# Optimization experiments

Hardware: AMD Instinct MI355X
Metric: run time of the kernel (lower is better)

## Reference

```python
import jax, jax.numpy as jnp
import numpy as np

K, Q, DIM = 64, 128, 1024
TF_W, DE_W, FFT_W = 1.0, 0.8, 0.6  # opt.TF_weight / DE_weight / FFT_weight


def setup_inputs() -> dict:
    key = jax.random.key(0)
    ks = jax.random.split(key, 9)
    def feats(k):
        return jax.random.normal(k, (K, Q, DIM), dtype=jnp.float32)
    def protos(k):
        return jax.random.normal(k, (K, DIM), dtype=jnp.float32)
    def var(k):
        # positive variances, bounded away from zero
        return jax.random.uniform(k, (K,), dtype=jnp.float32) + 0.5
    return {
        "TFq_output": feats(ks[0]), "TFs_proto": protos(ks[1]), "TF_variance": var(ks[2]),
        "DEq_output": feats(ks[3]), "DEs_proto": protos(ks[4]), "DE_variance": var(ks[5]),
        "FFTq_output": feats(ks[6]), "FFTs_proto": protos(ks[7]), "FFT_variance": var(ks[8]),
    }


def _mah_dist(xq, proto, variance):
    # ||x - p||^2 / var via expansion: avoids materializing (num, protonum, dim)
    x2 = jnp.sum(xq * xq, axis=1, keepdims=True)            # (num, 1)
    p2 = jnp.sum(proto * proto, axis=1)[None, :]            # (1, protonum)
    xp = xq @ proto.T                                       # (num, protonum)
    return (x2 - 2.0 * xp + p2) / variance[None, :]


def _modality(xq, proto, variance, w):
    logits = -_mah_dist(xq, proto, variance)
    pred = w * jax.nn.softmax(logits, axis=1)
    mahloss = -(w * jax.nn.log_softmax(logits, axis=1))
    return pred, mahloss


def reference(TFq_output, TFs_proto, TF_variance,
              DEq_output, DEs_proto, DE_variance,
              FFTq_output, FFTs_proto, FFT_variance):
    k, q, _ = TFq_output.shape
    y = jnp.repeat(jnp.arange(k), q)                         # (k*q,)

    tf_pred, tf_loss = _modality(TFq_output.reshape(k * q, -1), TFs_proto, TF_variance, TF_W)
    de_pred, de_loss = _modality(DEq_output.reshape(k * q, -1), DEs_proto, DE_variance, DE_W)
    fft_pred, fft_loss = _modality(FFTq_output.reshape(k * q, -1), FFTs_proto, FFT_variance, FFT_W)

    fusion_loss = tf_loss + de_loss + fft_loss               # (k*q, k)
    loss = jnp.take_along_axis(fusion_loss, y[:, None], axis=1).squeeze(-1).mean()

    pred_mah = tf_pred + de_pred + fft_pred
    pred = jnp.argmax(pred_mah, axis=1)
    acc = (pred == y).astype(jnp.float32).mean()
    return (loss, acc)
```

## Files before the change

kernel.cpp:

```cpp
#include <hip/hip_runtime.h>


typedef _Float16 half8 __attribute__((ext_vector_type(8)));
typedef float    floatx4 __attribute__((ext_vector_type(4)));

#define NCLS   64
#define QPC    128
#define DIM    1024
#define NROWS  (NCLS * QPC)
#define NRT    (NROWS / 16)

#define OFF_W      0
#define W_BYTES    (3 * NCLS * DIM * 2)
#define OFF_P2     W_BYTES
#define OFF_LP     (OFF_P2 + 3 * NCLS * 4)
#define OFF_CP     (OFF_LP + NRT * 4)
#define WS_NEED    (OFF_CP + NRT * 4)

__device__ __forceinline__ void dma16(const float* g, float* l) {
    __builtin_amdgcn_global_load_lds(
        (const __attribute__((address_space(1))) void*)g,
        (__attribute__((address_space(3))) void*)l,
        16, 0, 0);
}

__global__ __launch_bounds__(64) void prep_protos(
    const float* __restrict__ Ptf, const float* __restrict__ Pde,
    const float* __restrict__ Pff, _Float16* __restrict__ W,
    float* __restrict__ p2)
{
    const int m    = blockIdx.x >> 5;
    const int kcg  = blockIdx.x & 31;
    const int lane = threadIdx.x;
    const int l15  = lane & 15;
    const int quad = lane >> 4;
    const float* __restrict__ P = (m == 0) ? Ptf : (m == 1) ? Pde : Pff;

    #pragma unroll
    for (int t = 0; t < 4; ++t) {
        const float* src = P + (size_t)(t * 16 + l15) * DIM + kcg * 32 + quad * 8;
        const float4 b0 = *reinterpret_cast<const float4*>(src);
        const float4 b1 = *reinterpret_cast<const float4*>(src + 4);
        half8 h;
        h[0] = (_Float16)b0.x; h[1] = (_Float16)b0.y;
        h[2] = (_Float16)b0.z; h[3] = (_Float16)b0.w;
        h[4] = (_Float16)b1.x; h[5] = (_Float16)b1.y;
        h[6] = (_Float16)b1.z; h[7] = (_Float16)b1.w;
        *reinterpret_cast<half8*>(W + ((size_t)(m * 32 + kcg) * 4 + t) * 512 + lane * 8) = h;

        float s = b0.x*b0.x + b0.y*b0.y + b0.z*b0.z + b0.w*b0.w
                + b1.x*b1.x + b1.y*b1.y + b1.z*b1.z + b1.w*b1.w;
        s += __shfl_xor(s, 16);
        s += __shfl_xor(s, 32);
        if (quad == 0) atomicAdd(&p2[m * 64 + t * 16 + l15], s);
    }
}

__global__ __launch_bounds__(768, 6) void fusion_all(
    const float* __restrict__ Xtf, const float* __restrict__ Xde,
    const float* __restrict__ Xff,
    const float* __restrict__ Vtf, const float* __restrict__ Vde,
    const float* __restrict__ Vff,
    const _Float16* __restrict__ W, const float* __restrict__ p2g,
    float* __restrict__ lossPart,
    float* __restrict__ cntPart)
{
    __shared__ float buf[2][3][16][128];
    __shared__ float x2s[3][16];
    __shared__ float mxW[3][4][16];
    __shared__ float sW[3][4][16];
    __shared__ float predS[3][16][66];
    __shared__ float lossW[12];
    __shared__ float cntW[4];

    const int tid  = threadIdx.x;
    const int w    = tid >> 6;
    const int lane = tid & 63;
    const int l15  = lane & 15;
    const int quad = lane >> 4;
    const int m    = w >> 2;
    const int cq   = w & 3;
    const int rowBase = blockIdx.x * 16;

    const float* __restrict__ X = (m == 0) ? Xtf : (m == 1) ? Xde : Xff;
    const float* __restrict__ V = (m == 0) ? Vtf : (m == 1) ? Vde : Vff;
    const float  wgt = (m == 0) ? 1.0f : (m == 1) ? 0.8f : 0.6f;

    const int rl0 = cq * 4 + (lane >> 5);
    const int rl1 = rl0 + 2;
    const int sc0 = ((lane & 31) * 4) ^ ((rl0 & 7) * 4);
    const int sc1 = ((lane & 31) * 4) ^ ((rl1 & 7) * 4);
    const float* __restrict__ s0 = X + (size_t)(rowBase + rl0) * DIM + sc0;
    const float* __restrict__ s1 = X + (size_t)(rowBase + rl1) * DIM + sc1;

    const _Float16* __restrict__ wb = W + ((size_t)(m * 32) * 4 + cq) * 512 + lane * 8;

    floatx4 d = (floatx4){0.f, 0.f, 0.f, 0.f};
    float x2p = 0.0f;

    const int sw     = (l15 & 7) << 2;
    const int rowOff = l15 * 128;

    dma16(s0, &buf[0][m][cq * 4][0]);
    dma16(s1, &buf[0][m][cq * 4 + 2][0]);
    __syncthreads();

    #pragma unroll
    for (int c = 0; c < 8; ++c) {
        half8 bfr[4];
        #pragma unroll
        for (int kc = 0; kc < 4; ++kc)
            bfr[kc] = *reinterpret_cast<const half8*>(
                wb + (size_t)(c * 4 + kc) * 2048);
        asm volatile("" ::: "memory");

        if (c < 7) {
            dma16(s0 + (c + 1) * 128, &buf[(c + 1) & 1][m][cq * 4][0]);
            dma16(s1 + (c + 1) * 128, &buf[(c + 1) & 1][m][cq * 4 + 2][0]);
        }
        asm volatile("" ::: "memory");

        const float* tb = &buf[c & 1][m][0][0];
        #pragma unroll
        for (int kc = 0; kc < 4; ++kc) {
            const float4 a0 = *reinterpret_cast<const float4*>(
                tb + rowOff + kc * 32 + ((quad * 8) ^ sw));
            const float4 a1 = *reinterpret_cast<const float4*>(
                tb + rowOff + kc * 32 + (((quad * 8) + 4) ^ sw));

            if (cq == 0)
                x2p += a0.x*a0.x + a0.y*a0.y + a0.z*a0.z + a0.w*a0.w
                     + a1.x*a1.x + a1.y*a1.y + a1.z*a1.z + a1.w*a1.w;

            half8 af;
            af[0] = (_Float16)a0.x; af[1] = (_Float16)a0.y;
            af[2] = (_Float16)a0.z; af[3] = (_Float16)a0.w;
            af[4] = (_Float16)a1.x; af[5] = (_Float16)a1.y;
            af[6] = (_Float16)a1.z; af[7] = (_Float16)a1.w;

            d = __builtin_amdgcn_mfma_f32_16x16x32_f16(af, bfr[kc], d, 0, 0, 0);
        }
        __syncthreads();
    }

    if (cq == 0) {
        x2p += __shfl_xor(x2p, 16);
        x2p += __shfl_xor(x2p, 32);
        if (quad == 0) x2s[m][l15] = x2p;
    }
    __syncthreads();

    const int col = cq * 16 + l15;
    const float vc  = V[col];
    const float p2c = p2g[m * 64 + col];
    float lg[4];
    #pragma unroll
    for (int r = 0; r < 4; ++r)
        lg[r] = (2.0f * d[r] - x2s[m][quad * 4 + r] - p2c) / vc;

    #pragma unroll
    for (int r = 0; r < 4; ++r) {
        float mx = lg[r];
        #pragma unroll
        for (int dl = 1; dl <= 8; dl <<= 1) mx = fmaxf(mx, __shfl_xor(mx, dl));
        if (l15 == 0) mxW[m][cq][quad * 4 + r] = mx;
    }
    __syncthreads();

    float gmx[4];
    #pragma unroll
    for (int r = 0; r < 4; ++r) {
        const int row = quad * 4 + r;
        gmx[r] = fmaxf(fmaxf(mxW[m][0][row], mxW[m][1][row]),
                       fmaxf(mxW[m][2][row], mxW[m][3][row]));
        float s = expf(lg[r] - gmx[r]);
        #pragma unroll
        for (int dl = 1; dl <= 8; dl <<= 1) s += __shfl_xor(s, dl);
        if (l15 == 0) sW[m][cq][quad * 4 + r] = s;
    }
    __syncthreads();

    const int y = rowBase >> 7;
    float lossAcc = 0.0f;
    #pragma unroll
    for (int r = 0; r < 4; ++r) {
        const int row = quad * 4 + r;
        const float lse = gmx[r] + logf(sW[m][0][row] + sW[m][1][row]
                                      + sW[m][2][row] + sW[m][3][row]);
        if (col == y) lossAcc += wgt * (lse - lg[r]);
        predS[m][row][col] = wgt * expf(lg[r] - lse);
    }
    #pragma unroll
    for (int dl = 1; dl <= 32; dl <<= 1) lossAcc += __shfl_xor(lossAcc, dl);
    if (lane == 0) lossW[w] = lossAcc;
    __syncthreads();

    if (w < 4) {
        float cnt = 0.0f;
        #pragma unroll
        for (int r4 = 0; r4 < 4; ++r4) {
            const int row = w * 4 + r4;
            float bv = predS[0][row][lane] + predS[1][row][lane]
                     + predS[2][row][lane];
            int bc = lane;
            #pragma unroll
            for (int dl = 1; dl <= 32; dl <<= 1) {
                const float ov = __shfl_xor(bv, dl);
                const int   oc = __shfl_xor(bc, dl);
                if (ov > bv || (ov == bv && oc < bc)) { bv = ov; bc = oc; }
            }
            if (bc == y) cnt += 1.0f;
        }
        if (lane == 0) cntW[w] = cnt;
    }
    __syncthreads();

    if (tid == 0) {
        float L = 0.0f;
        #pragma unroll
        for (int i = 0; i < 12; ++i) L += lossW[i];
        lossPart[blockIdx.x] = L;
        cntPart[blockIdx.x]  = cntW[0] + cntW[1] + cntW[2] + cntW[3];
    }
}

__global__ __launch_bounds__(256) void finalize2(
    const float* __restrict__ lossPart, const float* __restrict__ cntPart,
    float* __restrict__ out)
{
    const int tid  = threadIdx.x;
    const int lane = tid & 63;
    const int v    = tid >> 6;
    float l = 0.0f, c = 0.0f;
    for (int i = tid; i < NRT; i += 256) l += lossPart[i];
    for (int i = tid; i < NRT; i += 256) c += cntPart[i];
    #pragma unroll
    for (int dl = 1; dl <= 32; dl <<= 1) {
        l += __shfl_xor(l, dl);
        c += __shfl_xor(c, dl);
    }
    __shared__ float sl[4], sc[4];
    if (lane == 0) { sl[v] = l; sc[v] = c; }
    __syncthreads();
    if (tid == 0) {
        out[0] = (sl[0] + sl[1] + sl[2] + sl[3]) * (1.0f / NROWS);
        out[1] = (sc[0] + sc[1] + sc[2] + sc[3]) * (1.0f / NROWS);
    }
}

#define NWAVES 12
#define KSPLIT 4
#define KSLICE (DIM / KSPLIT)
#define NITER  (KSLICE / 32)
#define DSTRIDE 17
#define PSTRIDE 65

__global__ __launch_bounds__(NWAVES * 64) void fusion_loss_fallback(
    const float* __restrict__ Xtf, const float* __restrict__ Ptf, const float* __restrict__ Vtf,
    const float* __restrict__ Xde, const float* __restrict__ Pde, const float* __restrict__ Vde,
    const float* __restrict__ Xff, const float* __restrict__ Pff, const float* __restrict__ Vff,
    float* __restrict__ out)
{
    __shared__ float dpart[NWAVES][64 * DSTRIDE];
    __shared__ float x2part[NWAVES][16];
    __shared__ float p2part[NWAVES][64];
    __shared__ float predL[16 * PSTRIDE];
    __shared__ float lossL;

    const int tid  = threadIdx.x;
    const int wave = tid >> 6;
    const int lane = tid & 63;
    const int l15  = lane & 15;
    const int quad = lane >> 4;
    const int m    = wave >> 2;
    const int kq   = wave & 3;
    const int rowBase = blockIdx.x * 16;

    for (int i = tid; i < 16 * PSTRIDE; i += NWAVES * 64) predL[i] = 0.0f;
    if (tid == 0) lossL = 0.0f;

    const float* __restrict__ X = (m == 0) ? Xtf : (m == 1) ? Xde : Xff;
    const float* __restrict__ P = (m == 0) ? Ptf : (m == 1) ? Pde : Pff;
    const float* __restrict__ V = (m == 0) ? Vtf : (m == 1) ? Vde : Vff;
    const float  w = (m == 0) ? 1.0f : (m == 1) ? 0.8f : 0.6f;

    floatx4 d[4];
    #pragma unroll
    for (int t = 0; t < 4; ++t) d[t] = (floatx4){0.f, 0.f, 0.f, 0.f};
    float x2p    = 0.0f;
    float p2p[4] = {0.f, 0.f, 0.f, 0.f};

    const float* xrow = X + (size_t)(rowBase + l15) * DIM + kq * KSLICE + quad * 8;
    const float* prow[4];
    #pragma unroll
    for (int t = 0; t < 4; ++t)
        prow[t] = P + (size_t)(t * 16 + l15) * DIM + kq * KSLICE + quad * 8;

    #pragma unroll 2
    for (int kc = 0; kc < NITER; ++kc) {
        const int ko = kc * 32;
        const float4 a0 = *reinterpret_cast<const float4*>(xrow + ko);
        const float4 a1 = *reinterpret_cast<const float4*>(xrow + ko + 4);
        float4 b0[4], b1[4];
        #pragma unroll
        for (int t = 0; t < 4; ++t) {
            b0[t] = *reinterpret_cast<const float4*>(prow[t] + ko);
            b1[t] = *reinterpret_cast<const float4*>(prow[t] + ko + 4);
        }
        x2p += a0.x*a0.x + a0.y*a0.y + a0.z*a0.z + a0.w*a0.w
             + a1.x*a1.x + a1.y*a1.y + a1.z*a1.z + a1.w*a1.w;
        half8 af;
        af[0] = (_Float16)a0.x; af[1] = (_Float16)a0.y;
        af[2] = (_Float16)a0.z; af[3] = (_Float16)a0.w;
        af[4] = (_Float16)a1.x; af[5] = (_Float16)a1.y;
        af[6] = (_Float16)a1.z; af[7] = (_Float16)a1.w;
        #pragma unroll
        for (int t = 0; t < 4; ++t) {
            p2p[t] += b0[t].x*b0[t].x + b0[t].y*b0[t].y + b0[t].z*b0[t].z + b0[t].w*b0[t].w
                    + b1[t].x*b1[t].x + b1[t].y*b1[t].y + b1[t].z*b1[t].z + b1[t].w*b1[t].w;
            half8 bf;
            bf[0] = (_Float16)b0[t].x; bf[1] = (_Float16)b0[t].y;
            bf[2] = (_Float16)b0[t].z; bf[3] = (_Float16)b0[t].w;
            bf[4] = (_Float16)b1[t].x; bf[5] = (_Float16)b1[t].y;
            bf[6] = (_Float16)b1[t].z; bf[7] = (_Float16)b1[t].w;
            d[t] = __builtin_amdgcn_mfma_f32_16x16x32_f16(af, bf, d[t], 0, 0, 0);
        }
    }

    x2p += __shfl_xor(x2p, 16);
    x2p += __shfl_xor(x2p, 32);
    #pragma unroll
    for (int t = 0; t < 4; ++t) {
        p2p[t] += __shfl_xor(p2p[t], 16);
        p2p[t] += __shfl_xor(p2p[t], 32);
    }
    {
        float* dp = &dpart[wave][lane * DSTRIDE];
        #pragma unroll
        for (int t = 0; t < 4; ++t)
            *reinterpret_cast<float4*>(dp + t * 4) =
                make_float4(d[t][0], d[t][1], d[t][2], d[t][3]);
        if (quad == 0) {
            x2part[wave][l15] = x2p;
            #pragma unroll
            for (int t = 0; t < 4; ++t) p2part[wave][t * 16 + l15] = p2p[t];
        }
    }
    __syncthreads();

    const int y = rowBase >> 7;

    if (kq == 0) {
        floatx4 dsum[4];
        #pragma unroll
        for (int t = 0; t < 4; ++t) dsum[t] = (floatx4){0.f, 0.f, 0.f, 0.f};
        float x2r[4] = {0.f, 0.f, 0.f, 0.f};
        float p2c[4] = {0.f, 0.f, 0.f, 0.f};
        #pragma unroll
        for (int k2 = 0; k2 < KSPLIT; ++k2) {
            const int wv = m * 4 + k2;
            const float* src = &dpart[wv][lane * DSTRIDE];
            #pragma unroll
            for (int t = 0; t < 4; ++t) {
                const float4 vv = *reinterpret_cast<const float4*>(src + t * 4);
                dsum[t][0] += vv.x; dsum[t][1] += vv.y; dsum[t][2] += vv.z; dsum[t][3] += vv.w;
            }
            #pragma unroll
            for (int r = 0; r < 4; ++r) x2r[r] += x2part[wv][quad * 4 + r];
            #pragma unroll
            for (int t = 0; t < 4; ++t) p2c[t] += p2part[wv][t * 16 + l15];
        }
        float vc[4];
        #pragma unroll
        for (int t = 0; t < 4; ++t) vc[t] = V[t * 16 + l15];

        float lossAcc = 0.0f;
        #pragma unroll
        for (int r = 0; r < 4; ++r) {
            float lg[4];
            #pragma unroll
            for (int t = 0; t < 4; ++t)
                lg[t] = (2.0f * dsum[t][r] - x2r[r] - p2c[t]) / vc[t];
            float mx = fmaxf(fmaxf(lg[0], lg[1]), fmaxf(lg[2], lg[3]));
            #pragma unroll
            for (int dl = 1; dl <= 8; dl <<= 1) mx = fmaxf(mx, __shfl_xor(mx, dl));
            float s = expf(lg[0] - mx) + expf(lg[1] - mx)
                    + expf(lg[2] - mx) + expf(lg[3] - mx);
            #pragma unroll
            for (int dl = 1; dl <= 8; dl <<= 1) s += __shfl_xor(s, dl);
            const float lse = mx + logf(s);
            const int row = quad * 4 + r;
            #pragma unroll
            for (int t = 0; t < 4; ++t) {
                const int colc = t * 16 + l15;
                if (colc == y) lossAcc += w * (lse - lg[t]);
                atomicAdd(&predL[row * PSTRIDE + colc], w * expf(lg[t] - lse));
            }
        }
        #pragma unroll
        for (int dl = 1; dl <= 32; dl <<= 1) lossAcc += __shfl_xor(lossAcc, dl);
        if (lane == 0) atomicAdd(&lossL, lossAcc);
    }
    __syncthreads();

    if (wave == 0) {
        float cnt = 0.0f;
        #pragma unroll 1
        for (int r = 0; r < 16; ++r) {
            float bv = predL[r * PSTRIDE + lane];
            int   bc = lane;
            #pragma unroll
            for (int dl = 1; dl <= 32; dl <<= 1) {
                const float ov = __shfl_xor(bv, dl);
                const int   oc = __shfl_xor(bc, dl);
                if (ov > bv || (ov == bv && oc < bc)) { bv = ov; bc = oc; }
            }
            if (lane == 0 && bc == y) cnt += 1.0f;
        }
        if (lane == 0) {
            atomicAdd(&out[0], lossL * (1.0f / NROWS));
            atomicAdd(&out[1], cnt * (1.0f / NROWS));
        }
    }
}

extern "C" void kernel_launch(void* const* d_in, const int* in_sizes, int n_in,
                              void* d_out, int out_size, void* d_ws, size_t ws_size,
                              hipStream_t stream) {
    const float* Xtf = (const float*)d_in[0];
    const float* Ptf = (const float*)d_in[1];
    const float* Vtf = (const float*)d_in[2];
    const float* Xde = (const float*)d_in[3];
    const float* Pde = (const float*)d_in[4];
    const float* Vde = (const float*)d_in[5];
    const float* Xff = (const float*)d_in[6];
    const float* Pff = (const float*)d_in[7];
    const float* Vff = (const float*)d_in[8];
    float* out = (float*)d_out;

    if (ws_size >= (size_t)WS_NEED) {
        char* ws = (char*)d_ws;
        _Float16* W     = (_Float16*)(ws + OFF_W);
        float*    p2    = (float*)(ws + OFF_P2);
        float*    lossP = (float*)(ws + OFF_LP);
        float*    cntP  = (float*)(ws + OFF_CP);

        hipMemsetAsync(p2, 0, 3 * NCLS * sizeof(float), stream);
        prep_protos<<<dim3(96), dim3(64), 0, stream>>>(Ptf, Pde, Pff, W, p2);
        fusion_all<<<dim3(NRT), dim3(768), 0, stream>>>(
            Xtf, Xde, Xff, Vtf, Vde, Vff, W, p2, lossP, cntP);
        finalize2<<<dim3(1), dim3(256), 0, stream>>>(lossP, cntP, out);
    } else {
        hipMemsetAsync(out, 0, 2 * sizeof(float), stream);
        fusion_loss_fallback<<<dim3(NROWS / 16), dim3(NWAVES * 64), 0, stream>>>(
            Xtf, Ptf, Vtf, Xde, Pde, Vde, Xff, Pff, Vff, out);
    }
}
```

Measured before the change: 150.9 us.

## Drop memset and finalize launch via last-block reduction and atomic-free prep

Removes the p2 memset by having each prep block reduce its row norms across waves in LDS and write them directly, and folds the finalize kernel into fusion_all using a done-counter where the last block sums the partial losses and counts. This cuts two launches/stream operations from the pipeline. It costs a threadfence plus atomic per block, and prep now runs with only 12 larger blocks, so it spreads across fewer CUs.

```diff
diff --git a/kernel.cpp b/kernel.cpp
--- a/kernel.cpp
+++ b/kernel.cpp
@@ -15,7 +15,8 @@
 #define OFF_P2     W_BYTES
 #define OFF_LP     (OFF_P2 + 3 * NCLS * 4)
 #define OFF_CP     (OFF_LP + NRT * 4)
-#define WS_NEED    (OFF_CP + NRT * 4)
+#define OFF_CNT    (OFF_CP + NRT * 4)
+#define WS_NEED    (OFF_CNT + 16)
 
 __device__ __forceinline__ void dma16(const float* g, float* l) {
     __builtin_amdgcn_global_load_lds(
@@ -24,23 +25,31 @@
         16, 0, 0);
 }
 
-__global__ __launch_bounds__(64) void prep_protos(
+__global__ __launch_bounds__(256) void prep_protos(
     const float* __restrict__ Ptf, const float* __restrict__ Pde,
     const float* __restrict__ Pff, _Float16* __restrict__ W,
-    float* __restrict__ p2)
+    float* __restrict__ p2, unsigned* __restrict__ doneCnt)
 {
-    const int m    = blockIdx.x >> 5;
-    const int kcg  = blockIdx.x & 31;
-    const int lane = threadIdx.x;
+    __shared__ float p2w[4][16];
+
+    const int m    = blockIdx.x >> 2;
+    const int t    = blockIdx.x & 3;
+    const int tid  = threadIdx.x;
+    const int v    = tid >> 6;
+    const int lane = tid & 63;
     const int l15  = lane & 15;
     const int quad = lane >> 4;
     const float* __restrict__ P = (m == 0) ? Ptf : (m == 1) ? Pde : Pff;
 
-    #pragma unroll
-    for (int t = 0; t < 4; ++t) {
-        const float* src = P + (size_t)(t * 16 + l15) * DIM + kcg * 32 + quad * 8;
-        const float4 b0 = *reinterpret_cast<const float4*>(src);
-        const float4 b1 = *reinterpret_cast<const float4*>(src + 4);
+    if (blockIdx.x == 0 && tid == 0) *doneCnt = 0u;
+
+    const float* src = P + (size_t)(t * 16 + l15) * DIM + quad * 8;
+    float s = 0.0f;
+    #pragma unroll
+    for (int i = 0; i < 8; ++i) {
+        const int kcg = v * 8 + i;
+        const float4 b0 = *reinterpret_cast<const float4*>(src + kcg * 32);
+        const float4 b1 = *reinterpret_cast<const float4*>(src + kcg * 32 + 4);
         half8 h;
         h[0] = (_Float16)b0.x; h[1] = (_Float16)b0.y;
         h[2] = (_Float16)b0.z; h[3] = (_Float16)b0.w;
@@ -48,12 +57,16 @@
         h[6] = (_Float16)b1.z; h[7] = (_Float16)b1.w;
         *reinterpret_cast<half8*>(W + ((size_t)(m * 32 + kcg) * 4 + t) * 512 + lane * 8) = h;
 
-        float s = b0.x*b0.x + b0.y*b0.y + b0.z*b0.z + b0.w*b0.w
-                + b1.x*b1.x + b1.y*b1.y + b1.z*b1.z + b1.w*b1.w;
-        s += __shfl_xor(s, 16);
-        s += __shfl_xor(s, 32);
-        if (quad == 0) atomicAdd(&p2[m * 64 + t * 16 + l15], s);
-    }
+        s += b0.x*b0.x + b0.y*b0.y + b0.z*b0.z + b0.w*b0.w
+           + b1.x*b1.x + b1.y*b1.y + b1.z*b1.z + b1.w*b1.w;
+    }
+    s += __shfl_xor(s, 16);
+    s += __shfl_xor(s, 32);
+    if (quad == 0) p2w[v][l15] = s;
+    __syncthreads();
+    if (v == 0 && quad == 0)
+        p2[m * 64 + t * 16 + l15] = p2w[0][l15] + p2w[1][l15]
+                                  + p2w[2][l15] + p2w[3][l15];
 }
 
 __global__ __launch_bounds__(768, 6) void fusion_all(
@@ -63,7 +76,9 @@
     const float* __restrict__ Vff,
     const _Float16* __restrict__ W, const float* __restrict__ p2g,
     float* __restrict__ lossPart,
-    float* __restrict__ cntPart)
+    float* __restrict__ cntPart,
+    unsigned* __restrict__ doneCnt,
+    float* __restrict__ out)
 {
     __shared__ float buf[2][3][16][128];
     __shared__ float x2s[3][16];
@@ -72,6 +87,8 @@
     __shared__ float predS[3][16][66];
     __shared__ float lossW[12];
     __shared__ float cntW[4];
+    __shared__ float redL[12], redC[12];
+    __shared__ unsigned lastFlag;
 
     const int tid  = threadIdx.x;
     const int w    = tid >> 6;
@@ -219,32 +236,35 @@
         float L = 0.0f;
         #pragma unroll
         for (int i = 0; i < 12; ++i) L += lossW[i];
-        lossPart[blockIdx.x] = L;
-        cntPart[blockIdx.x]  = cntW[0] + cntW[1] + cntW[2] + cntW[3];
-    }
-}
-
-__global__ __launch_bounds__(256) void finalize2(
-    const float* __restrict__ lossPart, const float* __restrict__ cntPart,
-    float* __restrict__ out)
-{
-    const int tid  = threadIdx.x;
-    const int lane = tid & 63;
-    const int v    = tid >> 6;
-    float l = 0.0f, c = 0.0f;
-    for (int i = tid; i < NRT; i += 256) l += lossPart[i];
-    for (int i = tid; i < NRT; i += 256) c += cntPart[i];
-    #pragma unroll
-    for (int dl = 1; dl <= 32; dl <<= 1) {
-        l += __shfl_xor(l, dl);
-        c += __shfl_xor(c, dl);
-    }
-    __shared__ float sl[4], sc[4];
-    if (lane == 0) { sl[v] = l; sc[v] = c; }
-    __syncthreads();
-    if (tid == 0) {
-        out[0] = (sl[0] + sl[1] + sl[2] + sl[3]) * (1.0f / NROWS);
-        out[1] = (sc[0] + sc[1] + sc[2] + sc[3]) * (1.0f / NROWS);
+        atomicExch(&lossPart[blockIdx.x], L);
+        atomicExch(&cntPart[blockIdx.x],
+                   cntW[0] + cntW[1] + cntW[2] + cntW[3]);
+        __threadfence();
+        lastFlag = ((atomicAdd(doneCnt, 1u) % NRT) == NRT - 1) ? 1u : 0u;
+    }
+    __syncthreads();
+
+    if (lastFlag) {
+        __threadfence();
+        float l = 0.0f, c = 0.0f;
+        for (int i = tid; i < NRT; i += 768) {
+            l += lossPart[i];
+            c += cntPart[i];
+        }
+        #pragma unroll
+        for (int dl = 1; dl <= 32; dl <<= 1) {
+            l += __shfl_xor(l, dl);
+            c += __shfl_xor(c, dl);
+        }
+        if (lane == 0) { redL[w] = l; redC[w] = c; }
+        __syncthreads();
+        if (tid == 0) {
+            float L = 0.0f, C = 0.0f;
+            #pragma unroll
+            for (int i = 0; i < 12; ++i) { L += redL[i]; C += redC[i]; }
+            out[0] = L * (1.0f / NROWS);
+            out[1] = C * (1.0f / NROWS);
+        }
     }
 }
 
@@ -444,12 +464,12 @@
         float*    p2    = (float*)(ws + OFF_P2);
         float*    lossP = (float*)(ws + OFF_LP);
         float*    cntP  = (float*)(ws + OFF_CP);
-
-        hipMemsetAsync(p2, 0, 3 * NCLS * sizeof(float), stream);
-        prep_protos<<<dim3(96), dim3(64), 0, stream>>>(Ptf, Pde, Pff, W, p2);
+        unsigned* cnt   = (unsigned*)(ws + OFF_CNT);
+
+        prep_protos<<<dim3(12), dim3(256), 0, stream>>>(
+            Ptf, Pde, Pff, W, p2, cnt);
         fusion_all<<<dim3(NRT), dim3(768), 0, stream>>>(
-            Xtf, Xde, Xff, Vtf, Vde, Vff, W, p2, lossP, cntP);
-        finalize2<<<dim3(1), dim3(256), 0, stream>>>(lossP, cntP, out);
+            Xtf, Xde, Xff, Vtf, Vde, Vff, W, p2, lossP, cntP, cnt, out);
     } else {
         hipMemsetAsync(out, 0, 2 * sizeof(float), stream);
         fusion_loss_fallback<<<dim3(NROWS / 16), dim3(NWAVES * 64), 0, stream>>>(
```

Result: slower. 163.2 us (+8.2%).
